# Optimization experiments

Measured on AMD Instinct MI355X. Metric: run time of the kernel, lower is better.

## Reference

```python
import jax, jax.numpy as jnp
import numpy as np

DIM = 512
HEADS = 8
DHEAD = 64
B, H, W = 4, 128, 128


def _dwconv(x, k):
    # x: (b, c, h, w), k: (c, 1, 3, 3) depthwise kernel (groups = c)
    return jax.lax.conv_general_dilated(
        x, k, window_strides=(1, 1), padding='SAME',
        dimension_numbers=('NCHW', 'OIHW', 'NCHW'),
        feature_group_count=x.shape[1])


def _l2norm(x, eps=1e-12):
    # torch F.normalize(p=2, dim=-1): x / clamp(||x||, eps)
    n = jnp.sqrt(jnp.sum(x * x, axis=-1, keepdims=True))
    return x / jnp.maximum(n, eps)


def setup_inputs() -> dict:
    key = jax.random.key(0)
    ks = jax.random.split(key, 10)
    s = 0.02
    return {
        'x_in': jax.random.normal(ks[0], (B, H, W, DIM), jnp.float32),
        'illu_fea_trans': jax.random.uniform(ks[1], (B, H, W, DIM), jnp.float32),
        'Wq': jax.random.normal(ks[2], (DIM, DIM), jnp.float32) * s,  # (out,in), no bias
        'Wk': jax.random.normal(ks[3], (DIM, DIM), jnp.float32) * s,
        'Wv': jax.random.normal(ks[4], (DIM, DIM), jnp.float32) * s,
        'rescale': jnp.ones((HEADS, 1, 1), jnp.float32),
        'Wp': jax.random.normal(ks[5], (DIM, DIM), jnp.float32) * s,  # proj weight (out,in)
        'bp': jnp.zeros((DIM,), jnp.float32),
        'pe1': jax.random.normal(ks[6], (DIM, 1, 3, 3), jnp.float32) * s,  # depthwise conv kernels
        'pe2': jax.random.normal(ks[7], (DIM, 1, 3, 3), jnp.float32) * s,
    }


def reference(x_in, illu_fea_trans, Wq, Wk, Wv, rescale, Wp, bp, pe1, pe2):
    b, h, w, c = x_in.shape
    n = h * w
    x = x_in.reshape(b, n, c)
    illu = illu_fea_trans.reshape(b, n, c)

    q = x @ Wq.T
    k = x @ Wk.T
    v = x @ Wv.T

    def to_heads_dn(t):  # (b, n, heads*d) -> (b, heads, d, n)
        return t.reshape(b, n, HEADS, DHEAD).transpose(0, 2, 3, 1)

    illu_h = illu.reshape(b, n, HEADS, DHEAD)
    v = ((v.reshape(b, n, HEADS, DHEAD)) * illu_h).transpose(0, 2, 3, 1)  # (b,heads,d,n)
    q = _l2norm(to_heads_dn(q))  # normalize along n
    k = _l2norm(to_heads_dn(k))

    # channel attention: (b,heads,d,d) score matrix
    attn = jnp.einsum('bhdn,bhen->bhde', k, q) * rescale
    attn = jax.nn.softmax(attn, axis=-1)
    xo = jnp.einsum('bhde,bhen->bhdn', attn, v)  # (b,heads,d,n)

    xo = xo.transpose(0, 3, 1, 2).reshape(b, n, HEADS * DHEAD)  # (b,n,c)
    out_c = (xo @ Wp.T + bp).reshape(b, h, w, c)

    # positional branch: depthwise conv -> GELU -> depthwise conv on v image
    v_img = v.reshape(b, HEADS * DHEAD, h, w)
    p = _dwconv(v_img, pe1)
    p = jax.nn.gelu(p, approximate=False)  # torch F.gelu default = erf
    p = _dwconv(p, pe2)
    out_p = p.transpose(0, 2, 3, 1)

    return out_c + out_p
```

## Files before the change

kernel.cpp:

```cpp
#include <hip/hip_runtime.h>
#include <hip/hip_bf16.h>
#include <math.h>

typedef __bf16 bf16;
typedef __attribute__((ext_vector_type(4))) __bf16 bf16x4;
typedef __attribute__((ext_vector_type(8))) __bf16 bf16x8;
typedef __attribute__((ext_vector_type(4))) float f32x4;

#define GLL(gp, lp) __builtin_amdgcn_global_load_lds( \
    (const __attribute__((address_space(1))) unsigned int*)(gp), \
    (__attribute__((address_space(3))) unsigned int*)(lp), 16, 0, 0)

#define WAIT_LGKM0() do { asm volatile("s_waitcnt lgkmcnt(0)" ::: "memory"); \
                          __builtin_amdgcn_sched_barrier(0); } while (0)
#define WAIT_VMC0() do { asm volatile("s_waitcnt vmcnt(0)" ::: "memory"); \
                         __builtin_amdgcn_sched_barrier(0); } while (0)


__device__ __forceinline__ bf16x8 cvt8(float4 a, float4 b) {
  bf16x8 o;
  o[0] = (bf16)a.x; o[1] = (bf16)a.y; o[2] = (bf16)a.z; o[3] = (bf16)a.w;
  o[4] = (bf16)b.x; o[5] = (bf16)b.y; o[6] = (bf16)b.z; o[7] = (bf16)b.w;
  return o;
}

__global__ __launch_bounds__(256) void prep_kernel(
    const float* __restrict__ x, const float* __restrict__ Wq,
    const float* __restrict__ Wk, const float* __restrict__ Wv,
    bf16* __restrict__ xb, bf16* __restrict__ wqkv,
    float* __restrict__ zattn, float* __restrict__ ssq, float* __restrict__ ssk)
{
  const long XG = 33554432L / 8;
  const long WG = 262144L / 8;
  long i = (long)blockIdx.x * 256 + threadIdx.x;
  if (i < XG) {
    const float4* xp = (const float4*)x;
    float4 a = xp[i * 2], b = xp[i * 2 + 1];
    *(bf16x8*)(xb + i * 8) = cvt8(a, b);
  } else if (i < XG + 3 * WG) {
    long j = i - XG;
    int w = (int)(j / WG);
    long r = j % WG;
    const float* src = (w == 0) ? Wq : ((w == 1) ? Wk : Wv);
    const float4* sp = (const float4*)src;
    float4 a = sp[r * 2], b = sp[r * 2 + 1];
    *(bf16x8*)(wqkv + (long)w * 262144 + r * 8) = cvt8(a, b);
  } else {
    long j = (i - XG - 3 * WG) * 8;
    float4 z = make_float4(0.f, 0.f, 0.f, 0.f);
    if (j < 131072) {
      *(float4*)(zattn + j) = z; *(float4*)(zattn + j + 4) = z;
    } else if (j < 133120) {
      long r = j - 131072; *(float4*)(ssq + r) = z; *(float4*)(ssq + r + 4) = z;
    } else {
      long r = j - 133120; *(float4*)(ssk + r) = z; *(float4*)(ssk + r + 4) = z;
    }
  }
}

__device__ __forceinline__ void gemm_tile_mainloop(
    const bf16* __restrict__ A, const bf16* __restrict__ B,
    int m0, int n0, bf16* As, bf16* Bs, f32x4 acc[4][4])
{
  int tid = threadIdx.x;
  int lane = tid & 63, wave = tid >> 6;
  int wy = wave >> 1, wx = wave & 1;
  int srow = tid >> 3;
  int scol = ((tid & 7) ^ (srow & 7)) * 8;
  const bf16* ag = A + ((size_t)(m0 + srow) << 9) + scol;
  const bf16* bg = B + ((size_t)(n0 + srow) << 9) + scol;
  bf16* lA = As + wave * 512;
  bf16* lB = Bs + wave * 512;
  int mloc = lane & 15;
  int kq = lane >> 4;

#pragma unroll
  for (int i = 0; i < 4; i++) {
    GLL(ag + i * 16384, lA + i * 2048);
    GLL(bg + i * 16384, lB + i * 2048);
  }
  __syncthreads();

#pragma unroll
  for (int k0 = 0; k0 < 512; k0 += 64) {
    int cur = (k0 >> 6) & 1;
    if (k0 + 64 < 512) {
      int nb = cur ^ 1;
#pragma unroll
      for (int i = 0; i < 4; i++) {
        GLL(ag + (k0 + 64) + i * 16384, lA + nb * 8192 + i * 2048);
        GLL(bg + (k0 + 64) + i * 16384, lB + nb * 8192 + i * 2048);
      }
    }
    const bf16* Ac = As + (cur << 13);
    const bf16* Bc = Bs + (cur << 13);
#pragma unroll
    for (int kh = 0; kh < 2; kh++) {
      bf16x8 af[4], bfr[4];
      int logical = kh * 4 + kq;
#pragma unroll
      for (int tt = 0; tt < 4; tt++) {
        int arow = wy * 64 + tt * 16 + mloc;
        af[tt] = *(const bf16x8*)&Ac[arow * 64 + (logical ^ (arow & 7)) * 8];
        int brow = wx * 64 + tt * 16 + mloc;
        bfr[tt] = *(const bf16x8*)&Bc[brow * 64 + (logical ^ (brow & 7)) * 8];
      }
#pragma unroll
      for (int ty = 0; ty < 4; ty++)
#pragma unroll
        for (int tx = 0; tx < 4; tx++)
          acc[ty][tx] = __builtin_amdgcn_mfma_f32_16x16x32_bf16(
              af[ty], bfr[tx], acc[ty][tx], 0, 0, 0);
    }
    __syncthreads();
  }
}

__global__ __launch_bounds__(256) void gemm_qkv_kernel(
    const bf16* __restrict__ xb, const bf16* __restrict__ wqkv,
    const float* __restrict__ illu,
    bf16* __restrict__ qbT, bf16* __restrict__ kbT, bf16* __restrict__ vb,
    float* __restrict__ ssq, float* __restrict__ ssk)
{
  __shared__ __align__(16) bf16 As[16384];
  __shared__ __align__(16) bf16 Bs[16384];
  int bid = blockIdx.x;
  int xcd = bid & 7, s = bid >> 3;
  int mt = xcd * 64 + s / 12, nt = s % 12;
  int m0 = mt * 128, n0 = nt * 128;
  f32x4 acc[4][4] = {};
  gemm_tile_mainloop(xb, wqkv, m0, n0, As, Bs, acc);

  int tid = threadIdx.x, lane = tid & 63, wave = tid >> 6;
  int wy = wave >> 1, wx = wave & 1;
  int r0 = m0 + wy * 64 + ((lane >> 4) << 2);
  int c0 = n0 + wx * 64 + (lane & 15);
  int region = n0 >> 9;
  if (region < 2) {
    bf16* outp = region ? kbT : qbT;
    float* dst = (region ? ssk : ssq) + (m0 >> 14) * 512;
    int bb = r0 >> 14;
    int nl0 = r0 & 16383;
#pragma unroll
    for (int tx = 0; tx < 4; tx++) {
      int lc = (c0 + tx * 16) & 511;
      bf16* colp = outp + (((size_t)bb << 23) + ((size_t)lc << 14));
      float ss = 0.f;
#pragma unroll
      for (int ty = 0; ty < 4; ty++) {
        f32x4 a = acc[ty][tx];
        ss += a[0] * a[0] + a[1] * a[1] + a[2] * a[2] + a[3] * a[3];
        bf16x4 o;
        o[0] = (bf16)a[0]; o[1] = (bf16)a[1]; o[2] = (bf16)a[2]; o[3] = (bf16)a[3];
        *(bf16x4*)&colp[nl0 + ty * 16] = o;
      }
      ss += __shfl_xor(ss, 16);
      ss += __shfl_xor(ss, 32);
      if ((lane >> 4) == 0) atomicAdd(dst + lc, ss);
    }
  } else {
#pragma unroll
    for (int tx = 0; tx < 4; tx++) {
      int lc = (c0 + tx * 16) & 511;
#pragma unroll
      for (int ty = 0; ty < 4; ty++) {
#pragma unroll
        for (int r = 0; r < 4; r++) {
          size_t idx = ((size_t)(r0 + ty * 16 + r) << 9) + lc;
          vb[idx] = (bf16)(acc[ty][tx][r] * illu[idx]);
        }
      }
    }
  }
}

__global__ __launch_bounds__(256) void attn_dots_kernel(
    const bf16* __restrict__ qbT, const bf16* __restrict__ kbT,
    float* __restrict__ attn)
{
  __shared__ __align__(16) bf16 ks[4][4096];
  __shared__ __align__(16) bf16 qs[4][4096];
  int bh = blockIdx.x, sp = blockIdx.y;
  int b = bh >> 3, h = bh & 7;
  int t = threadIdx.x, lane = t & 63, w = t >> 6;
  size_t base = ((size_t)b << 23) + ((size_t)h << 20);
  int n0 = sp * 1024 + w * 256;
  int srow = lane >> 3;
  int scol = ((lane & 7) ^ (srow & 7)) << 3;
  const bf16* kg = kbT + base + (size_t)srow * 16384 + n0 + scol;
  const bf16* qg = qbT + base + (size_t)srow * 16384 + n0 + scol;
  bf16* lk = &ks[w][0];
  bf16* lq = &qs[w][0];
  int mloc = lane & 15, kq = lane >> 4;
  f32x4 acc[4][4] = {};

  for (int it = 0; it < 4; ++it) {
    WAIT_LGKM0();
#pragma unroll
    for (int i = 0; i < 8; ++i) {
      GLL(kg + it * 64 + (size_t)i * 131072, lk + i * 512);
      GLL(qg + it * 64 + (size_t)i * 131072, lq + i * 512);
    }
    WAIT_VMC0();
    bf16x8 af[4][2], bfq[4][2];
#pragma unroll
    for (int tt = 0; tt < 4; ++tt) {
      int r = tt * 16 + mloc;
#pragma unroll
      for (int kh = 0; kh < 2; ++kh) {
        int slot = (kh * 4 + kq) ^ (r & 7);
        af[tt][kh]  = *(const bf16x8*)&lk[r * 64 + slot * 8];
        bfq[tt][kh] = *(const bf16x8*)&lq[r * 64 + slot * 8];
      }
    }
#pragma unroll
    for (int kh = 0; kh < 2; ++kh)
#pragma unroll
      for (int ta = 0; ta < 4; ++ta)
#pragma unroll
        for (int tb = 0; tb < 4; ++tb)
          acc[ta][tb] = __builtin_amdgcn_mfma_f32_16x16x32_bf16(
              af[ta][kh], bfq[tb][kh], acc[ta][tb], 0, 0, 0);
  }
  float* ap = attn + ((size_t)bh << 12);
  int rr = (lane >> 4) << 2, cc = lane & 15;
#pragma unroll
  for (int ta = 0; ta < 4; ++ta)
#pragma unroll
    for (int tb = 0; tb < 4; ++tb)
#pragma unroll
      for (int r = 0; r < 4; ++r)
        atomicAdd(&ap[(ta * 16 + rr + r) * 64 + tb * 16 + cc], acc[ta][tb][r]);
}

__global__ __launch_bounds__(64) void softmax_kernel(
    float* __restrict__ attn, const float* __restrict__ ssq,
    const float* __restrict__ ssk, const float* __restrict__ rescale)
{
  int bh = blockIdx.x, d = blockIdx.y;
  int b = bh >> 3, h = bh & 7;
  int e = threadIdx.x;
  float nq = fmaxf(sqrtf(ssq[b * 512 + h * 64 + e]), 1e-12f);
  float nk = fmaxf(sqrtf(ssk[b * 512 + h * 64 + d]), 1e-12f);
  float* ap = attn + ((size_t)bh << 12) + d * 64;
  float v = ap[e] * rescale[h] / (nk * nq);
  float m = v;
  for (int o = 32; o > 0; o >>= 1) m = fmaxf(m, __shfl_xor(m, o));
  float ex = expf(v - m);
  float s = ex;
  for (int o = 32; o > 0; o >>= 1) s += __shfl_xor(s, o);
  ap[e] = ex / s;
}

__global__ __launch_bounds__(256) void weff_kernel(
    const float* __restrict__ attn, const float* __restrict__ Wp,
    bf16* __restrict__ wefT)
{
  int cog = blockIdx.x, h = blockIdx.y, b = blockIdx.z;
  __shared__ float at[4096];
  __shared__ float wp[4096];
  int t = threadIdx.x;
  const float* ap = attn + ((size_t)(b * 8 + h) << 12);
  for (int i = t; i < 4096; i += 256) at[i] = ap[i];
  for (int i = t; i < 4096; i += 256) {
    int r = i >> 6, d = i & 63;
    wp[i] = Wp[((size_t)(cog * 64 + r) << 9) + h * 64 + d];
  }
  __syncthreads();
  int co_l = (t & 15) * 4, e_l = (t >> 4) * 4;
  float acc[16] = {0};
  for (int d = 0; d < 64; d++) {
    float w0 = wp[(co_l + 0) * 64 + d];
    float w1 = wp[(co_l + 1) * 64 + d];
    float w2 = wp[(co_l + 2) * 64 + d];
    float w3 = wp[(co_l + 3) * 64 + d];
    float4 av = *(const float4*)&at[d * 64 + e_l];
    acc[0]  += w0 * av.x; acc[1]  += w0 * av.y; acc[2]  += w0 * av.z; acc[3]  += w0 * av.w;
    acc[4]  += w1 * av.x; acc[5]  += w1 * av.y; acc[6]  += w1 * av.z; acc[7]  += w1 * av.w;
    acc[8]  += w2 * av.x; acc[9]  += w2 * av.y; acc[10] += w2 * av.z; acc[11] += w2 * av.w;
    acc[12] += w3 * av.x; acc[13] += w3 * av.y; acc[14] += w3 * av.z; acc[15] += w3 * av.w;
  }
#pragma unroll
  for (int i = 0; i < 4; i++)
#pragma unroll
    for (int j = 0; j < 4; j++)
      wefT[((size_t)b << 18) + ((size_t)(cog * 64 + co_l + i) << 9) + h * 64 + e_l + j] =
          (bf16)acc[i * 4 + j];
}

__global__ __launch_bounds__(256) void gemm_out_kernel(
    const bf16* __restrict__ vb, const bf16* __restrict__ wefT,
    const float* __restrict__ bp, float* __restrict__ out)
{
  __shared__ __align__(16) bf16 As[16384];
  __shared__ __align__(16) bf16 Bs[16384];
  int b = blockIdx.y;
  int bid = blockIdx.x;
  int xcd = bid & 7, s = bid >> 3;
  int mt = xcd * 16 + (s >> 2), nt = s & 3;
  int m0 = mt * 128, n0 = nt * 128;
  const bf16* A = vb + ((size_t)b << 23);
  const bf16* B = wefT + ((size_t)b << 18);
  f32x4 acc[4][4] = {};
  gemm_tile_mainloop(A, B, m0, n0, As, Bs, acc);

  int tid = threadIdx.x, lane = tid & 63, wave = tid >> 6;
  int wy = wave >> 1, wx = wave & 1;
  int r0 = (b << 14) + m0 + wy * 64 + ((lane >> 4) << 2);
  int c0 = n0 + wx * 64 + (lane & 15);
#pragma unroll
  for (int ty = 0; ty < 4; ty++) {
#pragma unroll
    for (int tx = 0; tx < 4; tx++) {
      int lc = c0 + tx * 16;
      float bias = bp[lc];
#pragma unroll
      for (int r = 0; r < 4; r++) {
        int grow = r0 + ty * 16 + r;
        out[((size_t)grow << 9) + lc] = acc[ty][tx][r] + bias;
      }
    }
  }
}

__global__ __launch_bounds__(256) void conv1_kernel(
    const bf16* __restrict__ vb, const float* __restrict__ pe1,
    bf16* __restrict__ pbuf)
{
  int b = blockIdx.y;
  int tile = blockIdx.x;
  int y0 = (tile >> 4) * 8, x0 = (tile & 15) * 8;
  int t = threadIdx.x;
  int cg = (t & 63) * 8, sp0 = t >> 6;
  float w[72];
#pragma unroll
  for (int i = 0; i < 8; i++)
#pragma unroll
    for (int k = 0; k < 9; k++)
      w[i * 9 + k] = pe1[(cg + i) * 9 + k];
  const bf16* vbase = vb + ((size_t)b << 23);
  bf16* pb = pbuf + ((size_t)b << 23);
  for (int s = sp0; s < 64; s += 4) {
    int y = y0 + (s >> 3), x = x0 + (s & 7);
    float a[8] = {0, 0, 0, 0, 0, 0, 0, 0};
#pragma unroll
    for (int ky = 0; ky < 3; ky++) {
      int yy = y + ky - 1;
      if (yy < 0 || yy >= 128) continue;
#pragma unroll
      for (int kx = 0; kx < 3; kx++) {
        int xx = x + kx - 1;
        if (xx < 0 || xx >= 128) continue;
        bf16x8 vv = *(const bf16x8*)&vbase[((size_t)(yy * 128 + xx) << 9) + cg];
#pragma unroll
        for (int i = 0; i < 8; i++) a[i] += (float)vv[i] * w[i * 9 + ky * 3 + kx];
      }
    }
    bf16x8 o;
#pragma unroll
    for (int i = 0; i < 8; i++) {
      float g = 0.5f * a[i] * (1.0f + erff(a[i] * 0.70710678118654752f));
      o[i] = (bf16)g;
    }
    *(bf16x8*)&pb[((size_t)(y * 128 + x) << 9) + cg] = o;
  }
}

__global__ __launch_bounds__(256) void conv2_kernel(
    const bf16* __restrict__ pbuf, const float* __restrict__ pe2,
    float* __restrict__ out)
{
  int b = blockIdx.y;
  int tile = blockIdx.x;
  int y0 = (tile >> 4) * 8, x0 = (tile & 15) * 8;
  int t = threadIdx.x;
  int cg = (t & 63) * 8, sp0 = t >> 6;
  float w[72];
#pragma unroll
  for (int i = 0; i < 8; i++)
#pragma unroll
    for (int k = 0; k < 9; k++)
      w[i * 9 + k] = pe2[(cg + i) * 9 + k];
  const bf16* pb = pbuf + ((size_t)b << 23);
  float* ob = out + ((size_t)b << 23);
  for (int s = sp0; s < 64; s += 4) {
    int y = y0 + (s >> 3), x = x0 + (s & 7);
    float a[8] = {0, 0, 0, 0, 0, 0, 0, 0};
#pragma unroll
    for (int ky = 0; ky < 3; ky++) {
      int yy = y + ky - 1;
      if (yy < 0 || yy >= 128) continue;
#pragma unroll
      for (int kx = 0; kx < 3; kx++) {
        int xx = x + kx - 1;
        if (xx < 0 || xx >= 128) continue;
        bf16x8 vv = *(const bf16x8*)&pb[((size_t)(yy * 128 + xx) << 9) + cg];
#pragma unroll
        for (int i = 0; i < 8; i++) a[i] += (float)vv[i] * w[i * 9 + ky * 3 + kx];
      }
    }
    size_t oi = ((size_t)(y * 128 + x) << 9) + cg;
    float4 o0 = *(float4*)&ob[oi];
    float4 o1 = *(float4*)&ob[oi + 4];
    o0.x += a[0]; o0.y += a[1]; o0.z += a[2]; o0.w += a[3];
    o1.x += a[4]; o1.y += a[5]; o1.z += a[6]; o1.w += a[7];
    *(float4*)&ob[oi] = o0;
    *(float4*)&ob[oi + 4] = o1;
  }
}

extern "C" void kernel_launch(void* const* d_in, const int* in_sizes, int n_in,
                              void* d_out, int out_size, void* d_ws, size_t ws_size,
                              hipStream_t stream) {
  (void)in_sizes; (void)n_in; (void)out_size; (void)ws_size;
  const float* x       = (const float*)d_in[0];
  const float* illu    = (const float*)d_in[1];
  const float* Wq      = (const float*)d_in[2];
  const float* Wk      = (const float*)d_in[3];
  const float* Wv      = (const float*)d_in[4];
  const float* rescale = (const float*)d_in[5];
  const float* Wp      = (const float*)d_in[6];
  const float* bp      = (const float*)d_in[7];
  const float* pe1     = (const float*)d_in[8];
  const float* pe2     = (const float*)d_in[9];
  float* out = (float*)d_out;
  char* ws = (char*)d_ws;

  bf16*  xb   = (bf16*)(ws);
  bf16*  wqkv = (bf16*)(ws + 67108864);
  bf16*  qbT  = (bf16*)(ws + 68681728);
  bf16*  kbT  = (bf16*)(ws + 135790592);
  bf16*  vb   = (bf16*)(ws + 202899456);
  float* ssq  = (float*)(ws + 270008320);
  float* ssk  = (float*)(ws + 270016512);
  float* attn = (float*)(ws + 270024704);
  bf16*  wefT = (bf16*)(ws + 270548992);
  bf16*  pbuf = xb;

  prep_kernel<<<16834, 256, 0, stream>>>(x, Wq, Wk, Wv, xb, wqkv, attn, ssq, ssk);
  gemm_qkv_kernel<<<6144, 256, 0, stream>>>(xb, wqkv, illu, qbT, kbT, vb, ssq, ssk);
  attn_dots_kernel<<<dim3(32, 16), 256, 0, stream>>>(qbT, kbT, attn);
  softmax_kernel<<<dim3(32, 64), 64, 0, stream>>>(attn, ssq, ssk, rescale);
  weff_kernel<<<dim3(8, 8, 4), 256, 0, stream>>>(attn, Wp, wefT);
  gemm_out_kernel<<<dim3(512, 4), 256, 0, stream>>>(vb, wefT, bp, out);
  conv1_kernel<<<dim3(256, 4), 256, 0, stream>>>(vb, pe1, pbuf);
  conv2_kernel<<<dim3(256, 4), 256, 0, stream>>>(pbuf, pe2, out);
}
```

Before: 810.7 us.

## Triple-buffer GEMM mainloop with BK=32 stages and raise occupancy

```diff
diff --git a/kernel.cpp b/kernel.cpp
--- a/kernel.cpp
+++ b/kernel.cpp
@@ -13,8 +13,9 @@
 
 #define WAIT_LGKM0() do { asm volatile("s_waitcnt lgkmcnt(0)" ::: "memory"); \
                           __builtin_amdgcn_sched_barrier(0); } while (0)
-#define WAIT_VMC0() do { asm volatile("s_waitcnt vmcnt(0)" ::: "memory"); \
+#define WAIT_VMC(n) do { asm volatile("s_waitcnt vmcnt(" #n ")" ::: "memory"); \
                          __builtin_amdgcn_sched_barrier(0); } while (0)
+#define BARRIER_FENCE() asm volatile("s_barrier" ::: "memory")
 
 
 __device__ __forceinline__ bf16x8 cvt8(float4 a, float4 b) {
@@ -65,8 +66,8 @@
   int tid = threadIdx.x;
   int lane = tid & 63, wave = tid >> 6;
   int wy = wave >> 1, wx = wave & 1;
-  int srow = tid >> 3;
-  int scol = ((tid & 7) ^ (srow & 7)) * 8;
+  int srow = tid >> 2;
+  int scol = ((tid & 3) ^ (srow & 3)) * 8;
   const bf16* ag = A + ((size_t)(m0 + srow) << 9) + scol;
   const bf16* bg = B + ((size_t)(n0 + srow) << 9) + scol;
   bf16* lA = As + wave * 512;
@@ -74,56 +75,55 @@
   int mloc = lane & 15;
   int kq = lane >> 4;
 
-#pragma unroll
-  for (int i = 0; i < 4; i++) {
-    GLL(ag + i * 16384, lA + i * 2048);
-    GLL(bg + i * 16384, lB + i * 2048);
-  }
-  __syncthreads();
-
-#pragma unroll
-  for (int k0 = 0; k0 < 512; k0 += 64) {
-    int cur = (k0 >> 6) & 1;
-    if (k0 + 64 < 512) {
-      int nb = cur ^ 1;
-#pragma unroll
-      for (int i = 0; i < 4; i++) {
-        GLL(ag + (k0 + 64) + i * 16384, lA + nb * 8192 + i * 2048);
-        GLL(bg + (k0 + 64) + i * 16384, lB + nb * 8192 + i * 2048);
-      }
-    }
-    const bf16* Ac = As + (cur << 13);
-    const bf16* Bc = Bs + (cur << 13);
-#pragma unroll
-    for (int kh = 0; kh < 2; kh++) {
-      bf16x8 af[4], bfr[4];
-      int logical = kh * 4 + kq;
-#pragma unroll
-      for (int tt = 0; tt < 4; tt++) {
-        int arow = wy * 64 + tt * 16 + mloc;
-        af[tt] = *(const bf16x8*)&Ac[arow * 64 + (logical ^ (arow & 7)) * 8];
-        int brow = wx * 64 + tt * 16 + mloc;
-        bfr[tt] = *(const bf16x8*)&Bc[brow * 64 + (logical ^ (brow & 7)) * 8];
-      }
-#pragma unroll
-      for (int ty = 0; ty < 4; ty++)
-#pragma unroll
-        for (int tx = 0; tx < 4; tx++)
-          acc[ty][tx] = __builtin_amdgcn_mfma_f32_16x16x32_bf16(
-              af[ty], bfr[tx], acc[ty][tx], 0, 0, 0);
-    }
-    __syncthreads();
-  }
-}
-
-__global__ __launch_bounds__(256) void gemm_qkv_kernel(
+#define STG(t) do { \
+    GLL(ag + (t) * 32,         lA + ((t) % 3) * 4096);        \
+    GLL(ag + (t) * 32 + 32768, lA + ((t) % 3) * 4096 + 2048); \
+    GLL(bg + (t) * 32,         lB + ((t) % 3) * 4096);        \
+    GLL(bg + (t) * 32 + 32768, lB + ((t) % 3) * 4096 + 2048); \
+  } while (0)
+
+  STG(0);
+  STG(1);
+  WAIT_VMC(4);
+  BARRIER_FENCE();
+
+#pragma unroll
+  for (int t = 0; t < 16; ++t) {
+    if (t + 2 < 16) STG(t + 2);
+    const bf16* Ac = As + (t % 3) * 4096;
+    const bf16* Bc = Bs + (t % 3) * 4096;
+    bf16x8 af[4], bfr[4];
+#pragma unroll
+    for (int tt = 0; tt < 4; tt++) {
+      int arow = wy * 64 + tt * 16 + mloc;
+      af[tt] = *(const bf16x8*)&Ac[arow * 32 + ((kq ^ (arow & 3)) << 3)];
+      int brow = wx * 64 + tt * 16 + mloc;
+      bfr[tt] = *(const bf16x8*)&Bc[brow * 32 + ((kq ^ (brow & 3)) << 3)];
+    }
+    WAIT_LGKM0();
+    __builtin_amdgcn_s_setprio(1);
+#pragma unroll
+    for (int ty = 0; ty < 4; ty++)
+#pragma unroll
+      for (int tx = 0; tx < 4; tx++)
+        acc[ty][tx] = __builtin_amdgcn_mfma_f32_16x16x32_bf16(
+            af[ty], bfr[tx], acc[ty][tx], 0, 0, 0);
+    __builtin_amdgcn_s_setprio(0);
+    if (t <= 13)      { WAIT_VMC(4); }
+    else if (t == 14) { WAIT_VMC(0); }
+    if (t < 15) BARRIER_FENCE();
+  }
+#undef STG
+}
+
+__global__ __launch_bounds__(256, 3) void gemm_qkv_kernel(
     const bf16* __restrict__ xb, const bf16* __restrict__ wqkv,
     const float* __restrict__ illu,
     bf16* __restrict__ qbT, bf16* __restrict__ kbT, bf16* __restrict__ vb,
     float* __restrict__ ssq, float* __restrict__ ssk)
 {
-  __shared__ __align__(16) bf16 As[16384];
-  __shared__ __align__(16) bf16 Bs[16384];
+  __shared__ __align__(16) bf16 As[12288];
+  __shared__ __align__(16) bf16 Bs[12288];
   int bid = blockIdx.x;
   int xcd = bid & 7, s = bid >> 3;
   int mt = xcd * 64 + s / 12, nt = s % 12;
@@ -201,7 +201,7 @@
       GLL(kg + it * 64 + (size_t)i * 131072, lk + i * 512);
       GLL(qg + it * 64 + (size_t)i * 131072, lq + i * 512);
     }
-    WAIT_VMC0();
+    WAIT_VMC(0);
     bf16x8 af[4][2], bfq[4][2];
 #pragma unroll
     for (int tt = 0; tt < 4; ++tt) {
@@ -288,12 +288,12 @@
           (bf16)acc[i * 4 + j];
 }
 
-__global__ __launch_bounds__(256) void gemm_out_kernel(
+__global__ __launch_bounds__(256, 3) void gemm_out_kernel(
     const bf16* __restrict__ vb, const bf16* __restrict__ wefT,
     const float* __restrict__ bp, float* __restrict__ out)
 {
-  __shared__ __align__(16) bf16 As[16384];
-  __shared__ __align__(16) bf16 Bs[16384];
+  __shared__ __align__(16) bf16 As[12288];
+  __shared__ __align__(16) bf16 Bs[12288];
   int b = blockIdx.y;
   int bid = blockIdx.x;
   int xcd = bid & 7, s = bid >> 3;
```

Result: faster. 783.0 us (-3.4%).
